# Kernel tuning notes

Measured on AMD Instinct MI355X. Metric: run time of the kernel, lower is better.

Reference implementation:

```python
import jax, jax.numpy as jnp
import numpy as np

N_POINTS = 200000
C_IN = 64
C_OUT = 64
K_VOL = 27  # 3x3x3 kernel offsets
N_PAIRS = 100000  # neighbor pairs per kernel offset
BN_EPS = 1e-5


def setup_inputs() -> dict:
    key = jax.random.key(0)
    k1, k2, k3, k4 = jax.random.split(key, 4)
    feats = jax.random.normal(k1, (N_POINTS, C_IN), dtype=jnp.float32)
    in_map = jax.random.randint(k2, (K_VOL, N_PAIRS), 0, N_POINTS, dtype=jnp.int32)
    out_map = jax.random.randint(k3, (K_VOL, N_PAIRS), 0, N_POINTS, dtype=jnp.int32)
    # learned params: conv kernel [K, Cin, Cout], BN affine + running stats
    kernel = jax.random.normal(k4, (K_VOL, C_IN, C_OUT), dtype=jnp.float32) * (1.0 / np.sqrt(C_IN * K_VOL))
    gamma = jnp.ones((C_OUT,), dtype=jnp.float32)
    beta = jnp.zeros((C_OUT,), dtype=jnp.float32)
    running_mean = jnp.zeros((C_OUT,), dtype=jnp.float32)
    running_var = jnp.ones((C_OUT,), dtype=jnp.float32)
    return {
        "feats": feats,
        "kernel": kernel,
        "gamma": gamma,
        "beta": beta,
        "running_mean": running_mean,
        "running_var": running_var,
        "in_map": in_map,
        "out_map": out_map,
    }


def reference(feats, kernel, gamma, beta, running_mean, running_var, in_map, out_map):
    # Sparse conv as gather -> per-offset GEMM -> scatter-add (torchsparse semantics)
    n = feats.shape[0]
    c_out = kernel.shape[-1]
    gathered = feats[in_map]                                   # [K, M, Cin]
    contrib = jnp.einsum('kmc,kco->kmo', gathered, kernel)     # [K, M, Cout]
    out = jnp.zeros((n, c_out), dtype=feats.dtype)
    out = out.at[out_map.reshape(-1)].add(contrib.reshape(-1, c_out))
    # BatchNorm (inference: fold running stats into scale/bias) + ReLU epilogue
    scale = gamma * jax.lax.rsqrt(running_var + BN_EPS)        # [Cout]
    out = out * scale + (beta - running_mean * scale)
    return jax.nn.relu(out)
```

## Files before the change

### kernel.cpp

```cpp
#include <hip/hip_runtime.h>
#include <hip/hip_bf16.h>

#define NPTS 200000
#define CIN 64
#define COUT 64
#define KVOL 27
#define NPAIRS 100000
#define GROUPS_PER_K (NPAIRS / 16)
#define GROUPS_PER_BLOCK 64
#define CHUNKS_PER_K ((GROUPS_PER_K + GROUPS_PER_BLOCK - 1) / GROUPS_PER_BLOCK)
#define BN_EPS 1e-5f

typedef __attribute__((ext_vector_type(8))) short short8;
typedef __attribute__((ext_vector_type(4))) float f32x4;

__device__ inline ushort f2bf(float x) {
    union { __hip_bfloat16 h; ushort u; } cv;
    cv.h = __float2bfloat16(x);
    return cv.u;
}

__global__ __launch_bounds__(256) void conv_scatter_kernel(
    const float* __restrict__ feats,
    const float* __restrict__ wk,
    const int* __restrict__ in_map,
    const int* __restrict__ out_map,
    float* __restrict__ accum)
{
    const int koff  = blockIdx.x / CHUNKS_PER_K;
    const int chunk = blockIdx.x % CHUNKS_PER_K;
    const int lane  = threadIdx.x & 63;
    const int wave  = threadIdx.x >> 6;
    const int m     = lane & 15;
    const int q     = lane >> 4;

    short8 bfrag[2][4];
    const float* wbase = wk + koff * (CIN * COUT);
    #pragma unroll
    for (int h = 0; h < 2; ++h) {
        #pragma unroll
        for (int nt = 0; nt < 4; ++nt) {
            #pragma unroll
            for (int e = 0; e < 8; ++e) {
                const int kin = h * 32 + q * 8 + e;
                bfrag[h][nt][e] = (short)f2bf(wbase[kin * COUT + nt * 16 + m]);
            }
        }
    }

    const int* imap = in_map + koff * NPAIRS;
    const int* omap = out_map + koff * NPAIRS;

    #pragma unroll 1
    for (int it = 0; it < GROUPS_PER_BLOCK / 4; ++it) {
        const int g = chunk * GROUPS_PER_BLOCK + it * 4 + wave;
        if (g >= GROUPS_PER_K) break;
        const int base = g * 16;

        const int row = imap[base + m];
        const float* fr = feats + row * CIN + q * 8;
        const f32x4 f00 = *(const f32x4*)(fr);
        const f32x4 f01 = *(const f32x4*)(fr + 4);
        const f32x4 f10 = *(const f32x4*)(fr + 32);
        const f32x4 f11 = *(const f32x4*)(fr + 36);

        short8 a0, a1;
        #pragma unroll
        for (int e = 0; e < 4; ++e) {
            a0[e]     = (short)f2bf(f00[e]);
            a0[e + 4] = (short)f2bf(f01[e]);
            a1[e]     = (short)f2bf(f10[e]);
            a1[e + 4] = (short)f2bf(f11[e]);
        }

        f32x4 acc[4];
        #pragma unroll
        for (int nt = 0; nt < 4; ++nt) acc[nt] = (f32x4){0.f, 0.f, 0.f, 0.f};
        #pragma unroll
        for (int nt = 0; nt < 4; ++nt) {
            acc[nt] = __builtin_amdgcn_mfma_f32_16x16x32_bf16(a0, bfrag[0][nt], acc[nt], 0, 0, 0);
            acc[nt] = __builtin_amdgcn_mfma_f32_16x16x32_bf16(a1, bfrag[1][nt], acc[nt], 0, 0, 0);
        }

        int orow[4];
        #pragma unroll
        for (int r = 0; r < 4; ++r) orow[r] = omap[base + q * 4 + r];

        #pragma unroll
        for (int nt = 0; nt < 4; ++nt) {
            #pragma unroll
            for (int r = 0; r < 4; ++r) {
                atomicAdd(accum + orow[r] * COUT + nt * 16 + m, acc[nt][r]);
            }
        }
    }
}

__global__ __launch_bounds__(256) void bn_relu_kernel(
    const float* __restrict__ accum,
    const float* __restrict__ gamma,
    const float* __restrict__ beta,
    const float* __restrict__ rmean,
    const float* __restrict__ rvar,
    float* __restrict__ out)
{
    __shared__ float s_scale[COUT];
    __shared__ float s_bias[COUT];
    if (threadIdx.x < COUT) {
        const int c = threadIdx.x;
        const float sc = gamma[c] * rsqrtf(rvar[c] + BN_EPS);
        s_scale[c] = sc;
        s_bias[c]  = beta[c] - rmean[c] * sc;
    }
    __syncthreads();

    const int idx = (blockIdx.x * 256 + threadIdx.x) * 4;
    if (idx < NPTS * COUT) {
        const f32x4 v = *(const f32x4*)(accum + idx);
        const int c0 = idx & (COUT - 1);
        f32x4 o;
        #pragma unroll
        for (int e = 0; e < 4; ++e) {
            o[e] = fmaxf(v[e] * s_scale[c0 + e] + s_bias[c0 + e], 0.f);
        }
        *(f32x4*)(out + idx) = o;
    }
}

extern "C" void kernel_launch(void* const* d_in, const int* in_sizes, int n_in,
                              void* d_out, int out_size, void* d_ws, size_t ws_size,
                              hipStream_t stream) {
    const float* feats = (const float*)d_in[0];
    const float* wk    = (const float*)d_in[1];
    const float* gamma = (const float*)d_in[2];
    const float* beta  = (const float*)d_in[3];
    const float* rmean = (const float*)d_in[4];
    const float* rvar  = (const float*)d_in[5];
    const int* imap    = (const int*)d_in[6];
    const int* omap    = (const int*)d_in[7];
    float* out         = (float*)d_out;
    float* accum       = (float*)d_ws;

    hipMemsetAsync(accum, 0, (size_t)NPTS * COUT * sizeof(float), stream);

    conv_scatter_kernel<<<KVOL * CHUNKS_PER_K, 256, 0, stream>>>(feats, wk, imap, omap, accum);

    bn_relu_kernel<<<(NPTS * COUT / 4 + 255) / 256, 256, 0, stream>>>(
        accum, gamma, beta, rmean, rvar, out);
}
```

Measured before the change: 676.9 us.

## Bucket neighbor pairs by output tile and accumulate in shared memory

Replaces the global-atomic scatter with a counting sort of all pairs into segments keyed by output block of 128 rows and kernel offset, built with a histogram, a prefix scan and a fill pass. Each conv block then owns 128 output rows, gathers its pairs, runs the MFMA GEMM per offset, accumulates into a swizzled LDS tile with shared atomics, and applies BN+ReLU in the same kernel. This removes the large accum memset, the global float atomics and the separate BN pass, at the cost of several extra preprocessing launches, global atomics during the sort, and one block per 128 rows that loops over all 27 offsets.

```diff
diff --git a/kernel.cpp b/kernel.cpp
--- a/kernel.cpp
+++ b/kernel.cpp
@@ -6,9 +6,12 @@
 #define COUT 64
 #define KVOL 27
 #define NPAIRS 100000
-#define GROUPS_PER_K (NPAIRS / 16)
-#define GROUPS_PER_BLOCK 64
-#define CHUNKS_PER_K ((GROUPS_PER_K + GROUPS_PER_BLOCK - 1) / GROUPS_PER_BLOCK)
+#define NTOT (KVOL * NPAIRS)
+#define RB 128
+#define NB ((NPTS + RB - 1) / RB)
+#define NSEG (NB * KVOL)
+#define SCAN_BLOCKS ((NSEG + 255) / 256)
+#define LIST_CAP (NTOT + NSEG * 15)
 #define BN_EPS 1e-5f
 
 typedef __attribute__((ext_vector_type(8))) short short8;
@@ -20,110 +23,191 @@
     return cv.u;
 }
 
-__global__ __launch_bounds__(256) void conv_scatter_kernel(
+
+__global__ __launch_bounds__(256) void hist_kernel(
+    const int* __restrict__ out_map, int* __restrict__ cnt)
+{
+    const int t = blockIdx.x * 256 + threadIdx.x;
+    if (t >= NTOT) return;
+    const int k = t / NPAIRS;
+    const int o = out_map[t];
+    atomicAdd(&cnt[(o >> 7) * KVOL + k], 1);
+}
+
+__global__ __launch_bounds__(256) void scan_block_kernel(
+    const int* __restrict__ cnt, int* __restrict__ off, int* __restrict__ bsum)
+{
+    __shared__ int s[256];
+    const int tid = threadIdx.x;
+    const int idx = blockIdx.x * 256 + tid;
+    const int v = (idx < NSEG) ? ((cnt[idx] + 15) & ~15) : 0;
+    s[tid] = v;
+    __syncthreads();
+    for (int d = 1; d < 256; d <<= 1) {
+        const int t = (tid >= d) ? s[tid - d] : 0;
+        __syncthreads();
+        s[tid] += t;
+        __syncthreads();
+    }
+    if (idx < NSEG) off[idx] = s[tid] - v;
+    if (tid == 255) bsum[blockIdx.x] = s[255];
+}
+
+__global__ __launch_bounds__(256) void scan_bsum_kernel(int* __restrict__ bsum)
+{
+    __shared__ int s[256];
+    const int tid = threadIdx.x;
+    const int v = (tid < SCAN_BLOCKS) ? bsum[tid] : 0;
+    s[tid] = v;
+    __syncthreads();
+    for (int d = 1; d < 256; d <<= 1) {
+        const int t = (tid >= d) ? s[tid - d] : 0;
+        __syncthreads();
+        s[tid] += t;
+        __syncthreads();
+    }
+    if (tid < SCAN_BLOCKS) bsum[tid] = s[tid] - v;
+}
+
+__global__ __launch_bounds__(256) void add_offsets_kernel(
+    int* __restrict__ off, const int* __restrict__ bsum)
+{
+    const int idx = blockIdx.x * 256 + threadIdx.x;
+    if (idx < NSEG) off[idx] += bsum[blockIdx.x];
+}
+
+__global__ __launch_bounds__(256) void fill_kernel(
+    const int* __restrict__ in_map, const int* __restrict__ out_map,
+    const int* __restrict__ off, int* __restrict__ cur, int* __restrict__ list)
+{
+    const int t = blockIdx.x * 256 + threadIdx.x;
+    if (t >= NTOT) return;
+    const int k = t / NPAIRS;
+    const int o = out_map[t];
+    const int seg = (o >> 7) * KVOL + k;
+    const int slot = atomicAdd(&cur[seg], 1);
+    list[off[seg] + slot] = in_map[t] | ((o & 127) << 18);
+}
+
+__global__ __launch_bounds__(256) void repack_w_kernel(
+    const float* __restrict__ wk, ushort* __restrict__ wpack)
+{
+    const int idx = blockIdx.x * 256 + threadIdx.x;
+    if (idx >= KVOL * 8 * 64 * 8) return;
+    const int e    = idx & 7;
+    const int lane = (idx >> 3) & 63;
+    const int f    = (idx >> 9) & 7;
+    const int k    = idx >> 12;
+    const int h = f >> 2, nt = f & 3;
+    const int q = lane >> 4, m = lane & 15;
+    const int kin = h * 32 + q * 8 + e;
+    wpack[idx] = f2bf(wk[k * (CIN * COUT) + kin * COUT + nt * 16 + m]);
+}
+
+__global__ __launch_bounds__(256) void conv_bucket_kernel(
     const float* __restrict__ feats,
-    const float* __restrict__ wk,
-    const int* __restrict__ in_map,
-    const int* __restrict__ out_map,
-    float* __restrict__ accum)
-{
-    const int koff  = blockIdx.x / CHUNKS_PER_K;
-    const int chunk = blockIdx.x % CHUNKS_PER_K;
-    const int lane  = threadIdx.x & 63;
-    const int wave  = threadIdx.x >> 6;
-    const int m     = lane & 15;
-    const int q     = lane >> 4;
-
-    short8 bfrag[2][4];
-    const float* wbase = wk + koff * (CIN * COUT);
-    #pragma unroll
-    for (int h = 0; h < 2; ++h) {
+    const ushort* __restrict__ wpack,
+    const int* __restrict__ off,
+    const int* __restrict__ cnt,
+    const int* __restrict__ list,
+    const float* __restrict__ gamma, const float* __restrict__ beta,
+    const float* __restrict__ rmean, const float* __restrict__ rvar,
+    float* __restrict__ out)
+{
+    __shared__ float sacc[RB * COUT];
+
+    const int b    = blockIdx.x;
+    const int tid  = threadIdx.x;
+    const int lane = tid & 63;
+    const int wave = tid >> 6;
+    const int m    = lane & 15;
+    const int q    = lane >> 4;
+
+    {
+        f32x4* z = (f32x4*)sacc;
         #pragma unroll
-        for (int nt = 0; nt < 4; ++nt) {
-            #pragma unroll
-            for (int e = 0; e < 8; ++e) {
-                const int kin = h * 32 + q * 8 + e;
-                bfrag[h][nt][e] = (short)f2bf(wbase[kin * COUT + nt * 16 + m]);
+        for (int i = 0; i < (RB * COUT / 4) / 256; ++i)
+            z[tid + i * 256] = (f32x4){0.f, 0.f, 0.f, 0.f};
+    }
+    __syncthreads();
+
+    #pragma unroll 1
+    for (int k = 0; k < KVOL; ++k) {
+        const int seg = b * KVOL + k;
+        const int s0  = off[seg];
+        const int ng  = (cnt[seg] + 15) >> 4;
+        if (ng == 0) continue;
+
+        short8 bfrag[2][4];
+        #pragma unroll
+        for (int f = 0; f < 8; ++f)
+            bfrag[f >> 2][f & 3] =
+                *(const short8*)(wpack + ((size_t)(k * 8 + f) * 64 + lane) * 8);
+
+        #pragma unroll 1
+        for (int g = wave; g < ng; g += 4) {
+            const int base = s0 + g * 16;
+            const int rec  = list[base + m];
+            const int row  = (rec >= 0) ? (rec & 0x3FFFF) : 0;
+
+            const float* fr = feats + (size_t)row * CIN + q * 8;
+            const f32x4 f00 = *(const f32x4*)(fr);
+            const f32x4 f01 = *(const f32x4*)(fr + 4);
+            const f32x4 f10 = *(const f32x4*)(fr + 32);
+            const f32x4 f11 = *(const f32x4*)(fr + 36);
+            short8 a0, a1;
+            #pragma unroll
+            for (int e = 0; e < 4; ++e) {
+                a0[e]     = (short)f2bf(f00[e]);
+                a0[e + 4] = (short)f2bf(f01[e]);
+                a1[e]     = (short)f2bf(f10[e]);
+                a1[e + 4] = (short)f2bf(f11[e]);
+            }
+
+            f32x4 acc[4];
+            #pragma unroll
+            for (int nt = 0; nt < 4; ++nt) acc[nt] = (f32x4){0.f, 0.f, 0.f, 0.f};
+            #pragma unroll
+            for (int nt = 0; nt < 4; ++nt) {
+                acc[nt] = __builtin_amdgcn_mfma_f32_16x16x32_bf16(a0, bfrag[0][nt], acc[nt], 0, 0, 0);
+                acc[nt] = __builtin_amdgcn_mfma_f32_16x16x32_bf16(a1, bfrag[1][nt], acc[nt], 0, 0, 0);
+            }
+
+            #pragma unroll
+            for (int r = 0; r < 4; ++r) {
+                const int rec_r = __shfl(rec, q * 4 + r);
+                if (rec_r >= 0) {
+                    const int loc = rec_r >> 18;
+                    const int sw  = (loc & 1) << 4;
+                    #pragma unroll
+                    for (int nt = 0; nt < 4; ++nt) {
+                        const int c = nt * 16 + m;
+                        atomicAdd(&sacc[loc * COUT + (c ^ sw)], acc[nt][r]);
+                    }
+                }
             }
         }
     }
-
-    const int* imap = in_map + koff * NPAIRS;
-    const int* omap = out_map + koff * NPAIRS;
-
-    #pragma unroll 1
-    for (int it = 0; it < GROUPS_PER_BLOCK / 4; ++it) {
-        const int g = chunk * GROUPS_PER_BLOCK + it * 4 + wave;
-        if (g >= GROUPS_PER_K) break;
-        const int base = g * 16;
-
-        const int row = imap[base + m];
-        const float* fr = feats + row * CIN + q * 8;
-        const f32x4 f00 = *(const f32x4*)(fr);
-        const f32x4 f01 = *(const f32x4*)(fr + 4);
-        const f32x4 f10 = *(const f32x4*)(fr + 32);
-        const f32x4 f11 = *(const f32x4*)(fr + 36);
-
-        short8 a0, a1;
+    __syncthreads();
+
+    const int loc = tid >> 1;
+    const int c0  = (tid & 1) * 32;
+    const int gr  = b * RB + loc;
+    if (gr < NPTS) {
+        const int sw = (loc & 1) << 4;
         #pragma unroll
-        for (int e = 0; e < 4; ++e) {
-            a0[e]     = (short)f2bf(f00[e]);
-            a0[e + 4] = (short)f2bf(f01[e]);
-            a1[e]     = (short)f2bf(f10[e]);
-            a1[e + 4] = (short)f2bf(f11[e]);
+        for (int cc = 0; cc < 32; cc += 4) {
+            const int c = c0 + cc;
+            const f32x4 v = *(const f32x4*)(&sacc[loc * COUT + (c ^ sw)]);
+            f32x4 o;
+            #pragma unroll
+            for (int e = 0; e < 4; ++e) {
+                const float sc = gamma[c + e] * rsqrtf(rvar[c + e] + BN_EPS);
+                const float bi = beta[c + e] - rmean[c + e] * sc;
+                o[e] = fmaxf(v[e] * sc + bi, 0.f);
+            }
+            *(f32x4*)(out + (size_t)gr * COUT + c) = o;
         }
-
-        f32x4 acc[4];
-        #pragma unroll
-        for (int nt = 0; nt < 4; ++nt) acc[nt] = (f32x4){0.f, 0.f, 0.f, 0.f};
-        #pragma unroll
-        for (int nt = 0; nt < 4; ++nt) {
-            acc[nt] = __builtin_amdgcn_mfma_f32_16x16x32_bf16(a0, bfrag[0][nt], acc[nt], 0, 0, 0);
-            acc[nt] = __builtin_amdgcn_mfma_f32_16x16x32_bf16(a1, bfrag[1][nt], acc[nt], 0, 0, 0);
-        }
-
-        int orow[4];
-        #pragma unroll
-        for (int r = 0; r < 4; ++r) orow[r] = omap[base + q * 4 + r];
-
-        #pragma unroll
-        for (int nt = 0; nt < 4; ++nt) {
-            #pragma unroll
-            for (int r = 0; r < 4; ++r) {
-                atomicAdd(accum + orow[r] * COUT + nt * 16 + m, acc[nt][r]);
-            }
-        }
-    }
-}
-
-__global__ __launch_bounds__(256) void bn_relu_kernel(
-    const float* __restrict__ accum,
-    const float* __restrict__ gamma,
-    const float* __restrict__ beta,
-    const float* __restrict__ rmean,
-    const float* __restrict__ rvar,
-    float* __restrict__ out)
-{
-    __shared__ float s_scale[COUT];
-    __shared__ float s_bias[COUT];
-    if (threadIdx.x < COUT) {
-        const int c = threadIdx.x;
-        const float sc = gamma[c] * rsqrtf(rvar[c] + BN_EPS);
-        s_scale[c] = sc;
-        s_bias[c]  = beta[c] - rmean[c] * sc;
-    }
-    __syncthreads();
-
-    const int idx = (blockIdx.x * 256 + threadIdx.x) * 4;
-    if (idx < NPTS * COUT) {
-        const f32x4 v = *(const f32x4*)(accum + idx);
-        const int c0 = idx & (COUT - 1);
-        f32x4 o;
-        #pragma unroll
-        for (int e = 0; e < 4; ++e) {
-            o[e] = fmaxf(v[e] * s_scale[c0 + e] + s_bias[c0 + e], 0.f);
-        }
-        *(f32x4*)(out + idx) = o;
     }
 }
 
@@ -139,12 +223,29 @@
     const int* imap    = (const int*)d_in[6];
     const int* omap    = (const int*)d_in[7];
     float* out         = (float*)d_out;
-    float* accum       = (float*)d_ws;
-
-    hipMemsetAsync(accum, 0, (size_t)NPTS * COUT * sizeof(float), stream);
-
-    conv_scatter_kernel<<<KVOL * CHUNKS_PER_K, 256, 0, stream>>>(feats, wk, imap, omap, accum);
-
-    bn_relu_kernel<<<(NPTS * COUT / 4 + 255) / 256, 256, 0, stream>>>(
-        accum, gamma, beta, rmean, rvar, out);
-}
+
+    char* ws = (char*)d_ws;
+    auto align1k = [](size_t x) { return (x + 1023) & ~(size_t)1023; };
+    size_t p = 0;
+    int* cnt      = (int*)(ws + p); p += align1k(NSEG * 4);
+    int* cur      = (int*)(ws + p); p += align1k(NSEG * 4);
+    int* off      = (int*)(ws + p); p += align1k(NSEG * 4);
+    int* bsum     = (int*)(ws + p); p += align1k(256 * 4);
+    ushort* wpack = (ushort*)(ws + p); p += align1k((size_t)KVOL * 8 * 64 * 8 * 2);
+    int* list     = (int*)(ws + p); p += align1k((size_t)LIST_CAP * 4);
+
+    hipMemsetAsync(cnt, 0, NSEG * 4, stream);
+    hipMemsetAsync(cur, 0, NSEG * 4, stream);
+    hipMemsetAsync(list, 0xFF, (size_t)LIST_CAP * 4, stream);
+
+    const int pb = (NTOT + 255) / 256;
+    hist_kernel<<<pb, 256, 0, stream>>>(omap, cnt);
+    scan_block_kernel<<<SCAN_BLOCKS, 256, 0, stream>>>(cnt, off, bsum);
+    scan_bsum_kernel<<<1, 256, 0, stream>>>(bsum);
+    add_offsets_kernel<<<SCAN_BLOCKS, 256, 0, stream>>>(off, bsum);
+    fill_kernel<<<pb, 256, 0, stream>>>(imap, omap, off, cur, list);
+    repack_w_kernel<<<(KVOL * 8 * 64 * 8 + 255) / 256, 256, 0, stream>>>(wk, wpack);
+
+    conv_bucket_kernel<<<NB, 256, 0, stream>>>(
+        feats, wpack, off, cnt, list, gamma, beta, rmean, rvar, out);
+}
```

After: 1.410 ms. +108.3%, slower.
